# Optimization experiments

Measured on AMD Instinct MI355X. Metric: run time of the kernel, lower is better.

## Reference

```python
import jax, jax.numpy as jnp
import numpy as np
from jax import lax

B, T, FEAT = 8, 512, 128
D_MODEL, D_STATE, D_INNER, DT_RANK = 128, 16, 256, 8
N_LAYERS, NUM_CLASSES = 10, 35
FLAT = 64 * (FEAT // 4)  # 2048


def setup_inputs():
    keys = iter(jax.random.split(jax.random.key(0), 48))
    def nrm(shape, s=0.05):
        return jax.random.normal(next(keys), shape, jnp.float32) * s
    inp = {}
    inp['x'] = jax.random.normal(next(keys), (B, T, FEAT), jnp.float32)
    inp['lengths'] = jax.random.randint(next(keys), (B,), 0, T)
    inp['conv_w1'] = nrm((32, 1, 3, 3)); inp['conv_b1'] = nrm((32,))
    inp['bn1_s'] = 1.0 + nrm((32,)); inp['bn1_b'] = nrm((32,))
    inp['conv_w2'] = nrm((32, 32, 3, 3)); inp['conv_b2'] = nrm((32,))
    inp['bn2_s'] = 1.0 + nrm((32,)); inp['bn2_b'] = nrm((32,))
    inp['conv_w3'] = nrm((64, 32, 3, 3)); inp['conv_b3'] = nrm((64,))
    inp['bn3_s'] = 1.0 + nrm((64,)); inp['bn3_b'] = nrm((64,))
    inp['conv_w4'] = nrm((64, 64, 3, 3)); inp['conv_b4'] = nrm((64,))
    inp['bn4_s'] = 1.0 + nrm((64,)); inp['bn4_b'] = nrm((64,))
    inp['proj_w'] = nrm((D_MODEL, FLAT), 0.02); inp['proj_b'] = nrm((D_MODEL,))
    inp['proj_ln_s'] = jnp.ones((D_MODEL,)); inp['proj_ln_b'] = jnp.zeros((D_MODEL,))
    L = N_LAYERS
    inp['blk_ln_s'] = jnp.ones((L, D_MODEL)); inp['blk_ln_b'] = jnp.zeros((L, D_MODEL))
    inp['in_w'] = nrm((L, 2 * D_INNER, D_MODEL))
    inp['cw'] = nrm((L, D_INNER, 4)); inp['cb'] = nrm((L, D_INNER))
    inp['xp_w'] = nrm((L, DT_RANK + 2 * D_STATE, D_INNER))
    inp['dt_w'] = nrm((L, D_INNER, DT_RANK))
    inp['dt_b'] = nrm((L, D_INNER)) - 4.0  # softplus(-4) ~ 0.018: realistic small dt
    inp['A_log'] = jnp.tile(jnp.log(jnp.arange(1, D_STATE + 1, dtype=jnp.float32))[None, None, :], (L, D_INNER, 1))
    inp['Dp'] = jnp.ones((L, D_INNER))
    inp['out_w'] = nrm((L, D_MODEL, D_INNER))
    inp['pre_ln_s'] = jnp.ones((D_MODEL,)); inp['pre_ln_b'] = jnp.zeros((D_MODEL,))
    inp['cls_w1'] = nrm((D_MODEL // 2, D_MODEL)); inp['cls_b1'] = nrm((D_MODEL // 2,))
    inp['cls_w2'] = nrm((NUM_CLASSES, D_MODEL // 2)); inp['cls_b2'] = nrm((NUM_CLASSES,))
    return inp


def _ln(x, s, b):
    m = jnp.mean(x, -1, keepdims=True)
    v = jnp.mean((x - m) ** 2, -1, keepdims=True)
    return (x - m) * lax.rsqrt(v + 1e-5) * s + b


def _conv2d(x, w, b):
    y = lax.conv_general_dilated(x, w, (1, 1), 'SAME', dimension_numbers=('NCHW', 'OIHW', 'NCHW'))
    return y + b[None, :, None, None]


def _bn(x, s, b):  # eval-mode BatchNorm folded to per-channel affine
    return x * s[None, :, None, None] + b[None, :, None, None]


def _pool(x, kh, kw):
    return lax.reduce_window(x, -jnp.inf, lax.max, (1, 1, kh, kw), (1, 1, kh, kw), 'VALID')


def _mamba(x, in_w, cw, cb, xp_w, dt_w, dt_b, A_log, Dp, out_w):
    bb = x.shape[0]
    xz = jnp.einsum('btd,ed->bte', x, in_w)                  # [B,T,2*d_inner]
    xm, z = jnp.split(xz, 2, axis=-1)
    # causal depthwise conv1d (torch pads both sides by 3 then truncates to T == left-pad 3)
    xc = lax.conv_general_dilated(xm.transpose(0, 2, 1), cw[:, None, :], (1,), [(3, 0)],
                                  dimension_numbers=('NCH', 'OIH', 'NCH'), feature_group_count=D_INNER)
    xc = jax.nn.silu(xc + cb[None, :, None]).transpose(0, 2, 1)  # [B,T,d_inner]
    dbc = jnp.einsum('btd,ed->bte', xc, xp_w)
    dt, Bm, Cm = jnp.split(dbc, [DT_RANK, DT_RANK + D_STATE], axis=-1)
    dt = jax.nn.softplus(jnp.einsum('btr,dr->btd', dt, dt_w) + dt_b)  # [B,T,d_inner]
    A = -jnp.exp(A_log)                                      # [d_inner,d_state]
    dA = jnp.exp(dt[..., None] * A)                          # [B,T,d,n]
    dBu = (dt * xc)[..., None] * Bm[:, :, None, :]           # [B,T,d,n]
    def step(h, inp):
        dA_t, dBu_t, C_t = inp
        h = dA_t * h + dBu_t
        return h, jnp.einsum('bdn,bn->bd', h, C_t)
    h0 = jnp.zeros((bb, D_INNER, D_STATE), x.dtype)
    _, ys = lax.scan(step, h0, (dA.transpose(1, 0, 2, 3), dBu.transpose(1, 0, 2, 3), Cm.transpose(1, 0, 2)))
    y = ys.transpose(1, 0, 2) + Dp * xc
    y = y * jax.nn.silu(z)
    return jnp.einsum('btd,ed->bte', y, out_w)


def _forward(x, lengths, conv_w1, conv_b1, bn1_s, bn1_b, conv_w2, conv_b2, bn2_s, bn2_b,
             conv_w3, conv_b3, bn3_s, bn3_b, conv_w4, conv_b4, bn4_s, bn4_b,
             proj_w, proj_b, proj_ln_s, proj_ln_b, blk_ln_s, blk_ln_b,
             in_w, cw, cb, xp_w, dt_w, dt_b, A_log, Dp, out_w,
             pre_ln_s, pre_ln_b, cls_w1, cls_b1, cls_w2, cls_b2):
    h = x.transpose(0, 2, 1)[:, None]                        # [B,1,F,T]
    h = jax.nn.silu(_bn(_conv2d(h, conv_w1, conv_b1), bn1_s, bn1_b))
    h = jax.nn.silu(_bn(_conv2d(h, conv_w2, conv_b2), bn2_s, bn2_b))
    h = _pool(h, 2, 2)
    h = jax.nn.silu(_bn(_conv2d(h, conv_w3, conv_b3), bn3_s, bn3_b))
    h = jax.nn.silu(_bn(_conv2d(h, conv_w4, conv_b4), bn4_s, bn4_b))
    h = _pool(h, 2, 1)                                       # [B,64,F/4,T/2]
    h = h.transpose(0, 3, 1, 2).reshape(h.shape[0], h.shape[3], -1)  # [B,T',64*F/4]
    h = jax.nn.silu(_ln(jnp.einsum('btf,df->btd', h, proj_w) + proj_b, proj_ln_s, proj_ln_b))
    for i in range(N_LAYERS):
        h = h + _mamba(_ln(h, blk_ln_s[i], blk_ln_b[i]), in_w[i], cw[i], cb[i], xp_w[i],
                       dt_w[i], dt_b[i], A_log[i], Dp[i], out_w[i])
    h = _ln(h, pre_ln_s, pre_ln_b)
    t_lens = jnp.clip(lengths // 2, 1)
    mask = (jnp.arange(h.shape[1])[None, :] < t_lens[:, None]).astype(h.dtype)[..., None]
    pooled = (h * mask).sum(1) / jnp.clip(mask.sum(1), 1.0)
    c = jax.nn.silu(jnp.einsum('bd,hd->bh', pooled, cls_w1) + cls_b1)
    return jnp.einsum('bh,ch->bc', c, cls_w2) + cls_b2


def reference(x, lengths, conv_w1, conv_b1, bn1_s, bn1_b, conv_w2, conv_b2, bn2_s, bn2_b,
              conv_w3, conv_b3, bn3_s, bn3_b, conv_w4, conv_b4, bn4_s, bn4_b,
              proj_w, proj_b, proj_ln_s, proj_ln_b, blk_ln_s, blk_ln_b,
              in_w, cw, cb, xp_w, dt_w, dt_b, A_log, Dp, out_w,
              pre_ln_s, pre_ln_b, cls_w1, cls_b1, cls_w2, cls_b2):
    return _forward(x, lengths, conv_w1, conv_b1, bn1_s, bn1_b, conv_w2, conv_b2, bn2_s, bn2_b,
                    conv_w3, conv_b3, bn3_s, bn3_b, conv_w4, conv_b4, bn4_s, bn4_b,
                    proj_w, proj_b, proj_ln_s, proj_ln_b, blk_ln_s, blk_ln_b,
                    in_w, cw, cb, xp_w, dt_w, dt_b, A_log, Dp, out_w,
                    pre_ln_s, pre_ln_b, cls_w1, cls_b1, cls_w2, cls_b2)
```

## Files before the change

### kernel.cpp

```cpp
#include <hip/hip_runtime.h>
#include <math.h>

#define B_ 8
#define T_ 512
#define FEAT_ 128
#define TP 256
#define DM 128
#define DI 256
#define DS 16
#define DTR 8
#define NL 10

__device__ __forceinline__ float fsilu(float x){ return x / (1.f + __expf(-x)); }
__device__ __forceinline__ float fsoftplus(float x){ return (x > 20.f) ? x : log1pf(__expf(x)); }

__global__ void k_transpose_x(const float* __restrict__ x, float* __restrict__ xT){
  int idx = blockIdx.x*256 + threadIdx.x;
  if(idx >= B_*FEAT_*T_) return;
  int t = idx % T_; int f = (idx/T_) % FEAT_; int b = idx/(T_*FEAT_);
  xT[idx] = x[((size_t)b*T_ + t)*FEAT_ + f];
}

__device__ __forceinline__ void wt_one(const float* __restrict__ w, float* __restrict__ o,
                                       int idx, int CO, int CIN){
  int k = idx % 9; int ci = (idx/9) % CIN; int co = idx/(9*CIN);
  o[((size_t)(ci*(CO>>3) + (co>>3)))*72 + (co&7)*9 + k] = w[idx];
}
__global__ void k_wt_all(const float* __restrict__ w1, const float* __restrict__ w2,
                         const float* __restrict__ w3, const float* __restrict__ w4,
                         float* __restrict__ o1, float* __restrict__ o2,
                         float* __restrict__ o3, float* __restrict__ o4){
  int idx = blockIdx.x*256 + threadIdx.x;
  if(idx < 288){ wt_one(w1, o1, idx, 32, 1); return; }
  idx -= 288;
  if(idx < 9216){ wt_one(w2, o2, idx, 32, 32); return; }
  idx -= 9216;
  if(idx < 18432){ wt_one(w3, o3, idx, 64, 32); return; }
  idx -= 18432;
  if(idx < 36864){ wt_one(w4, o4, idx, 64, 64); return; }
}

template<int CIN, int CO, int CPW, int CIG, int COG>
__global__ __launch_bounds__(256) void k_conv_t4(const float* __restrict__ in,
     const float* __restrict__ wt, const float* __restrict__ cb,
     const float* __restrict__ bs, const float* __restrict__ bb,
     float* __restrict__ out, int H, int W){
  constexpr int NS = CO/CPW;
  __shared__ __align__(16) float tile[CIG*360];
  int tid = threadIdx.x;
  int lane = tid & 63;
  int wav = __builtin_amdgcn_readfirstlane(tid >> 6);
  int wpr = W >> 4, hpr = H >> 4;
  int idx = blockIdx.x;
  int cog = idx % COG; idx /= COG;
  int tj = idx % wpr; idx /= wpr;
  int ti = idx % hpr; int b = idx / hpr;
  int i0 = ti*16, j0 = tj*16;
  int r = lane & 15, cg = lane >> 4;
  int wslot = cog*4 + wav;
  const float* wbase = wt + (size_t)wslot*72;
  float acc[CPW][4] = {};
  for(int cig = 0; cig < CIN; cig += CIG){
    __syncthreads();
    for(int u = tid; u < CIG*324; u += 256){
      int ci = u / 324; int rem = u - ci*324; int rr = rem / 18; int cc = rem - rr*18;
      int gi = i0 - 1 + rr, gj = j0 - 1 + cc;
      float v = 0.f;
      if(gi >= 0 && gi < H && gj >= 0 && gj < W)
        v = in[((size_t)(b*CIN + cig + ci)*H + gi)*W + gj];
      tile[ci*360 + rr*20 + cc] = v;
    }
    __syncthreads();
    for(int ci = 0; ci < CIG; ci++){
      const float4* wp4 = (const float4*)(wbase + (size_t)(cig+ci)*(NS*72));
      float4 w4q[18];
      #pragma unroll
      for(int q=0;q<18;q++) w4q[q] = wp4[q];
      const float* wf = (const float*)w4q;
      #pragma unroll
      for(int kh=0;kh<3;kh++){
        float4 a = *(const float4*)&tile[ci*360 + (r+kh)*20 + cg*4];
        float4 bv = *(const float4*)&tile[ci*360 + (r+kh)*20 + cg*4 + 4];
        float v[6] = {a.x,a.y,a.z,a.w,bv.x,bv.y};
        #pragma unroll
        for(int co=0;co<CPW;co++){
          #pragma unroll
          for(int kw=0;kw<3;kw++){
            float wv = wf[co*9 + kh*3 + kw];
            #pragma unroll
            for(int u2=0;u2<4;u2++)
              acc[co][u2] = fmaf(wv, v[kw+u2], acc[co][u2]);
          }
        }
      }
    }
  }
  int i = i0 + r;
  #pragma unroll
  for(int co=0; co<CPW; co++){
    int c = cog*(4*CPW) + wav*CPW + co;
    float s = bs[c], bias = cb[c]*s + bb[c];
    float4 o;
    o.x = fsilu(acc[co][0]*s + bias);
    o.y = fsilu(acc[co][1]*s + bias);
    o.z = fsilu(acc[co][2]*s + bias);
    o.w = fsilu(acc[co][3]*s + bias);
    *(float4*)&out[((size_t)(b*CO + c)*H + i)*W + j0 + cg*4] = o;
  }
}

__global__ void k_pool2x2(const float* __restrict__ in, float* __restrict__ out,
                          int C, int Hi, int Wi){
  int Ho = Hi>>1, Wo = Wi>>1;
  int total = B_*C*Ho*Wo;
  int idx = blockIdx.x*256 + threadIdx.x;
  if(idx >= total) return;
  int j = idx % Wo; int i = (idx/Wo)%Ho; int c = (idx/(Wo*Ho))%C; int b = idx/(Wo*Ho*C);
  const float* p = in + (((size_t)(b*C+c)*Hi + 2*i)*Wi + 2*j);
  out[idx] = fmaxf(fmaxf(p[0], p[1]), fmaxf(p[Wi], p[Wi+1]));
}

__global__ __launch_bounds__(256) void k_proj(const float* __restrict__ R0,
    const float* __restrict__ W, float* __restrict__ pbuf){
  __shared__ __align__(16) float As[16][33];
  __shared__ __align__(16) float Ws[16][68];
  int tid = threadIdx.x;
  int n0 = blockIdx.x*64, m0 = blockIdx.y*32;
  int kc = blockIdx.z;
  int b = m0 >> 8;
  int t_base = m0 & 255;
  int tx = tid&15, ty = tid>>4;
  float acc[2][4] = {};
  for(int k0=0; k0<256; k0+=16){
    int kg0 = kc*256 + k0;
    if(tid < 128){
      int row = tid>>2, cq = (tid&3)*4;
      #pragma unroll
      for(int c2=0;c2<4;c2++){
        int k = kg0 + cq + c2;
        int c = k>>5, hh = k&31;
        const float* p = R0 + (((size_t)(b*64+c)*64 + 2*hh)*256 + t_base + row);
        As[cq+c2][row] = fmaxf(p[0], p[256]);
      }
    } else {
      int u = tid - 128; int n = u>>1, cq = (u&1)*8;
      const float* wp = W + (size_t)(n0+n)*2048 + kg0 + cq;
      float4 v0 = *(const float4*)wp, v1 = *(const float4*)(wp+4);
      Ws[cq+0][n]=v0.x; Ws[cq+1][n]=v0.y; Ws[cq+2][n]=v0.z; Ws[cq+3][n]=v0.w;
      Ws[cq+4][n]=v1.x; Ws[cq+5][n]=v1.y; Ws[cq+6][n]=v1.z; Ws[cq+7][n]=v1.w;
    }
    __syncthreads();
    #pragma unroll
    for(int kk=0;kk<16;kk++){
      float a0 = As[kk][ty*2+0];
      float a1 = As[kk][ty*2+1];
      float4 w4 = *(const float4*)&Ws[kk][tx*4];
      float wv4[4] = {w4.x,w4.y,w4.z,w4.w};
      #pragma unroll
      for(int j=0;j<4;j++){
        acc[0][j] = fmaf(a0, wv4[j], acc[0][j]);
        acc[1][j] = fmaf(a1, wv4[j], acc[1][j]);
      }
    }
    __syncthreads();
  }
  float* pb = pbuf + (size_t)kc*2048*DM;
  #pragma unroll
  for(int iu=0;iu<2;iu++){
    int m = m0 + ty*2 + iu;
    #pragma unroll
    for(int j=0;j<4;j++){
      int n = n0 + tx*4 + j;
      pb[(size_t)m*DM + n] = acc[iu][j];
    }
  }
}

__global__ void k_lnp(const float* __restrict__ pbuf, const float* __restrict__ bias,
                      const float* __restrict__ g, const float* __restrict__ b,
                      float* __restrict__ out){
  int row = blockIdx.x;
  int t = threadIdx.x;
  float v0 = bias[t], v1 = bias[t+64];
  #pragma unroll
  for(int kc=0;kc<8;kc++){
    const float* p = pbuf + ((size_t)kc*2048 + row)*DM;
    v0 += p[t]; v1 += p[t+64];
  }
  float s = v0 + v1;
  #pragma unroll
  for(int m=32;m>=1;m>>=1) s += __shfl_xor(s, m);
  float mean = s * (1.f/128.f);
  float e0 = v0-mean, e1 = v1-mean;
  float q = e0*e0 + e1*e1;
  #pragma unroll
  for(int m=32;m>=1;m>>=1) q += __shfl_xor(q, m);
  float inv = rsqrtf(q*(1.f/128.f) + 1e-5f);
  float o0 = fsilu(e0*inv*g[t] + b[t]);
  float o1 = fsilu(e1*inv*g[t+64] + b[t+64]);
  float* po = out + (size_t)row*DM;
  po[t] = o0; po[t+64] = o1;
}

template<int SILU>
__global__ void k_ln(const float* __restrict__ in, const float* __restrict__ g,
                     const float* __restrict__ b, float* __restrict__ out){
  int row = blockIdx.x;
  int t = threadIdx.x;
  const float* p = in + (size_t)row*DM;
  float v0 = p[t], v1 = p[t+64];
  float s = v0 + v1;
  #pragma unroll
  for(int m=32;m>=1;m>>=1) s += __shfl_xor(s, m);
  float mean = s * (1.f/128.f);
  float e0 = v0-mean, e1 = v1-mean;
  float q = e0*e0 + e1*e1;
  #pragma unroll
  for(int m=32;m>=1;m>>=1) q += __shfl_xor(q, m);
  float inv = rsqrtf(q*(1.f/128.f) + 1e-5f);
  float o0 = e0*inv*g[t] + b[t];
  float o1 = e1*inv*g[t+64] + b[t+64];
  if(SILU){ o0 = fsilu(o0); o1 = fsilu(o1); }
  float* po = out + (size_t)row*DM;
  po[t] = o0; po[t+64] = o1;
}

__global__ __launch_bounds__(256) void k_lnxz(const float* __restrict__ hbuf,
    const float* __restrict__ g, const float* __restrict__ bb,
    const float* __restrict__ W, float* __restrict__ out){
  __shared__ __align__(16) float lns[32][132];
  __shared__ __align__(16) float Ws[16][68];
  int tid = threadIdx.x;
  int n0 = blockIdx.x*64, m0 = blockIdx.y*32;
  for(int u=tid; u<1024; u+=256){
    int row = u>>5, c4 = (u&31)*4;
    float4 v = *(const float4*)(hbuf + (size_t)(m0+row)*DM + c4);
    lns[row][c4] = v.x; lns[row][c4+1] = v.y; lns[row][c4+2] = v.z; lns[row][c4+3] = v.w;
  }
  __syncthreads();
  {
    int lane = tid & 63, wv = tid >> 6;
    for(int rr = wv; rr < 32; rr += 4){
      float v0 = lns[rr][lane], v1 = lns[rr][lane+64];
      float s = v0+v1;
      #pragma unroll
      for(int mm=32;mm>=1;mm>>=1) s += __shfl_xor(s,mm);
      float mean = s*(1.f/128.f);
      float e0 = v0-mean, e1 = v1-mean;
      float q = e0*e0+e1*e1;
      #pragma unroll
      for(int mm=32;mm>=1;mm>>=1) q += __shfl_xor(q,mm);
      float inv = rsqrtf(q*(1.f/128.f)+1e-5f);
      lns[rr][lane]    = e0*inv*g[lane] + bb[lane];
      lns[rr][lane+64] = e1*inv*g[lane+64] + bb[lane+64];
    }
  }
  __syncthreads();
  int tx = tid&15, ty = tid>>4;
  float acc[2][4] = {};
  for(int k0=0;k0<128;k0+=16){
    {
      int n = tid>>2, c4 = (tid&3)*4;
      float4 v = *(const float4*)(W + (size_t)(n0+n)*DM + k0 + c4);
      Ws[c4+0][n]=v.x; Ws[c4+1][n]=v.y; Ws[c4+2][n]=v.z; Ws[c4+3][n]=v.w;
    }
    __syncthreads();
    #pragma unroll
    for(int kk=0;kk<16;kk++){
      float a0 = lns[ty*2+0][k0+kk];
      float a1 = lns[ty*2+1][k0+kk];
      float4 w4 = *(const float4*)&Ws[kk][tx*4];
      float wv4[4] = {w4.x,w4.y,w4.z,w4.w};
      #pragma unroll
      for(int j=0;j<4;j++){
        acc[0][j] = fmaf(a0, wv4[j], acc[0][j]);
        acc[1][j] = fmaf(a1, wv4[j], acc[1][j]);
      }
    }
    __syncthreads();
  }
  #pragma unroll
  for(int iu=0;iu<2;iu++){
    int m = m0 + ty*2 + iu;
    float* po = out + (size_t)m*512 + n0 + tx*4;
    #pragma unroll
    for(int j=0;j<4;j++) po[j] = acc[iu][j];
  }
}

__global__ __launch_bounds__(256) void k_xproj8(const float* __restrict__ xz,
    const float* __restrict__ cw, const float* __restrict__ cb,
    const float* __restrict__ xpw, const float* __restrict__ dtw,
    const float* __restrict__ dtb_, float* __restrict__ xc_g,
    float* __restrict__ dbc_g, float* __restrict__ dt_g){
  __shared__ float xzs[11][64];
  __shared__ float As[64][9];
  __shared__ float Wp[64][41];
  __shared__ float dtin[8][9];
  __shared__ float dtw_s[256][9];
  int tid = threadIdx.x;
  int row0 = blockIdx.x*8; int b = row0 >> 8; int t0 = row0 & 255;
  int rA = tid & 7, cgA = tid >> 3;
  int dlC = tid & 63, rqC = tid >> 6;
  float acc0 = 0.f, acc1 = 0.f;
  for(int ch=0; ch<4; ch++){
    int d0 = ch*64;
    __syncthreads();
    for(int u=tid; u<11*64; u+=256){
      int rr = u>>6, dl = u&63;
      int t = t0 + rr - 3;
      xzs[rr][dl] = (t >= 0) ? xz[((size_t)(b*TP)+t)*512 + d0 + dl] : 0.f;
    }
    for(int u=tid; u<40*64; u+=256){
      int nn = u>>6, dk = u&63;
      Wp[dk][nn] = xpw[(size_t)nn*DI + d0 + dk];
    }
    __syncthreads();
    {
      float cw0 = cw[(d0+dlC)*4+0], cw1 = cw[(d0+dlC)*4+1];
      float cw2 = cw[(d0+dlC)*4+2], cw3 = cw[(d0+dlC)*4+3];
      float cbv = cb[d0+dlC];
      #pragma unroll
      for(int i=0;i<2;i++){
        int rr = rqC*2 + i;
        float a = cbv;
        a = fmaf(cw0, xzs[rr+0][dlC], a);
        a = fmaf(cw1, xzs[rr+1][dlC], a);
        a = fmaf(cw2, xzs[rr+2][dlC], a);
        a = fmaf(cw3, xzs[rr+3][dlC], a);
        float v = fsilu(a);
        As[dlC][rr] = v;
        xc_g[((size_t)row0 + rr)*DI + d0 + dlC] = v;
      }
    }
    __syncthreads();
    for(int dk=0; dk<64; dk++){
      float a = As[dk][rA];
      acc0 = fmaf(a, Wp[dk][cgA], acc0);
      if(cgA < 8) acc1 = fmaf(a, Wp[dk][cgA+32], acc1);
    }
  }
  if(cgA < 8){
    dtin[rA][cgA] = acc0;
    dbc_g[((size_t)row0 + rA)*40 + cgA + 32] = acc1;
  } else {
    dbc_g[((size_t)row0 + rA)*40 + cgA] = acc0;
  }
  for(int u=tid; u<256*8; u+=256) dtw_s[u>>3][u&7] = dtw[u];
  __syncthreads();
  {
    int d = tid;
    float bias = dtb_[d];
    float w8[8];
    #pragma unroll
    for(int k=0;k<8;k++) w8[k] = dtw_s[d][k];
    #pragma unroll
    for(int r2=0;r2<8;r2++){
      float a = bias;
      #pragma unroll
      for(int k=0;k<8;k++) a = fmaf(dtin[r2][k], w8[k], a);
      dt_g[((size_t)row0 + r2)*DI + d] = fsoftplus(a);
    }
  }
}

__global__ __launch_bounds__(1024) void k_scan3(const float* __restrict__ dtb,
      const float* __restrict__ xc, const float* __restrict__ xz,
      const float* __restrict__ dbc, const float* __restrict__ A_log,
      const float* __restrict__ Dp, float* __restrict__ y){
  __shared__ float dt_s[TP][8], xc_s[TP][8];
  __shared__ float Bs[TP][16], Cs[TP][16];
  __shared__ float Eb[8][128], Pb[8][128];
  int tid = threadIdx.x;
  int c = tid >> 7, gl = (tid >> 4) & 7, n = tid & 15;
  int dblk = blockIdx.x & 31, b = blockIdx.x >> 5;
  int d0 = dblk*8;
  size_t rbase = (size_t)b*TP;
  for(int u=tid; u<TP*8; u+=1024){
    int tt = u>>3, gg = u&7;
    size_t r = rbase + tt;
    dt_s[tt][gg] = dtb[r*DI + d0 + gg];
    xc_s[tt][gg] = xc [r*DI + d0 + gg];
  }
  for(int u=tid; u<TP*16; u+=1024){
    int tt = u>>4, nn = u&15;
    size_t r = rbase + tt;
    Bs[tt][nn] = dbc[r*40 + 8  + nn];
    Cs[tt][nn] = dbc[r*40 + 24 + nn];
  }
  __syncthreads();
  int d = d0 + gl;
  float An = -__expf(A_log[d*DS + n]);
  float h = 0.f, dtsum = 0.f;
  int tA = c*32;
  float yloc[32], ev[32];
  #pragma unroll
  for(int i=0;i<32;i++){
    int t = tA + i;
    float dtv = dt_s[t][gl];
    dtsum += dtv;
    float e = __expf(dtv*An);
    ev[i] = e;
    h = fmaf(e, h, dtv*xc_s[t][gl]*Bs[t][n]);
    float p = h*Cs[t][n];
    p += __shfl_xor(p,1); p += __shfl_xor(p,2);
    p += __shfl_xor(p,4); p += __shfl_xor(p,8);
    yloc[i] = p;
  }
  Eb[c][gl*16+n] = h;
  Pb[c][gl*16+n] = __expf(An*dtsum);
  __syncthreads();
  float g = 0.f;
  for(int cp=0; cp<c; cp++)
    g = fmaf(Pb[cp][gl*16+n], g, Eb[cp][gl*16+n]);
  float Dpd = Dp[d];
  #pragma unroll
  for(int i=0;i<32;i++){
    int t = tA + i;
    g *= ev[i];
    float p = g*Cs[t][n];
    p += __shfl_xor(p,1); p += __shfl_xor(p,2);
    p += __shfl_xor(p,4); p += __shfl_xor(p,8);
    if(n==0){
      float zv = xz[(rbase+t)*512 + DI + d];
      float xcv = xc_s[t][gl];
      y[(rbase+t)*DI + d] = (yloc[i] + p + Dpd*xcv) * fsilu(zv);
    }
  }
}

__global__ __launch_bounds__(256) void k_out16(const float* __restrict__ A,
    const float* __restrict__ W, float* __restrict__ C){
  __shared__ float As[16][17];
  __shared__ __align__(16) float Ws[16][68];
  int tid = threadIdx.x;
  int n0 = blockIdx.x*64, m0 = blockIdx.y*16;
  int tx = tid&15, ty = tid>>4;
  float acc[4] = {};
  for(int k0=0;k0<256;k0+=16){
    {
      int row = tid>>4, kk = tid&15;
      As[kk][row] = A[(size_t)(m0+row)*DI + k0 + kk];
    }
    {
      int n = tid>>2, cq = (tid&3)*4;
      float4 v = *(const float4*)(W + (size_t)(n0+n)*DI + k0 + cq);
      Ws[cq+0][n]=v.x; Ws[cq+1][n]=v.y; Ws[cq+2][n]=v.z; Ws[cq+3][n]=v.w;
    }
    __syncthreads();
    #pragma unroll
    for(int kk=0;kk<16;kk++){
      float a0 = As[kk][ty];
      float4 w4 = *(const float4*)&Ws[kk][tx*4];
      acc[0] = fmaf(a0, w4.x, acc[0]);
      acc[1] = fmaf(a0, w4.y, acc[1]);
      acc[2] = fmaf(a0, w4.z, acc[2]);
      acc[3] = fmaf(a0, w4.w, acc[3]);
    }
    __syncthreads();
  }
  int m = m0 + ty;
  float* cp = &C[(size_t)m*DM + n0 + tx*4];
  cp[0] += acc[0]; cp[1] += acc[1]; cp[2] += acc[2]; cp[3] += acc[3];
}

__global__ void k_head(const float* __restrict__ hln, const int* __restrict__ lengths,
                       const float* __restrict__ w1, const float* __restrict__ b1,
                       const float* __restrict__ w2, const float* __restrict__ b2,
                       float* __restrict__ out){
  __shared__ float pooled[DM];
  __shared__ float cbuf[64];
  int b = blockIdx.x, tid = threadIdx.x;
  int tl = lengths[b] >> 1; if(tl < 1) tl = 1;
  float s = 0.f;
  const float* p = hln + (size_t)b*TP*DM + tid;
  for(int t=0;t<tl;t++) s += p[(size_t)t*DM];
  pooled[tid] = s / (float)tl;
  __syncthreads();
  if(tid < 64){
    float a = b1[tid];
    const float* wp = w1 + tid*DM;
    for(int k=0;k<DM;k++) a = fmaf(pooled[k], wp[k], a);
    cbuf[tid] = fsilu(a);
  }
  __syncthreads();
  if(tid < 35){
    float a = b2[tid];
    const float* wp = w2 + tid*64;
    for(int k=0;k<64;k++) a = fmaf(cbuf[k], wp[k], a);
    out[b*35+tid] = a;
  }
}

extern "C" void kernel_launch(void* const* d_in, const int* in_sizes, int n_in,
                              void* d_out, int out_size, void* d_ws, size_t ws_size,
                              hipStream_t stream){
  (void)in_sizes; (void)n_in; (void)out_size; (void)ws_size;
  const float* x        = (const float*)d_in[0];
  const int*   lengths  = (const int*)  d_in[1];
  const float* conv_w1  = (const float*)d_in[2];  const float* conv_b1 = (const float*)d_in[3];
  const float* bn1_s    = (const float*)d_in[4];  const float* bn1_b   = (const float*)d_in[5];
  const float* conv_w2  = (const float*)d_in[6];  const float* conv_b2 = (const float*)d_in[7];
  const float* bn2_s    = (const float*)d_in[8];  const float* bn2_b   = (const float*)d_in[9];
  const float* conv_w3  = (const float*)d_in[10]; const float* conv_b3 = (const float*)d_in[11];
  const float* bn3_s    = (const float*)d_in[12]; const float* bn3_b   = (const float*)d_in[13];
  const float* conv_w4  = (const float*)d_in[14]; const float* conv_b4 = (const float*)d_in[15];
  const float* bn4_s    = (const float*)d_in[16]; const float* bn4_b   = (const float*)d_in[17];
  const float* proj_w   = (const float*)d_in[18]; const float* proj_b  = (const float*)d_in[19];
  const float* proj_ln_s= (const float*)d_in[20]; const float* proj_ln_b=(const float*)d_in[21];
  const float* blk_ln_s = (const float*)d_in[22]; const float* blk_ln_b =(const float*)d_in[23];
  const float* in_w     = (const float*)d_in[24];
  const float* cw       = (const float*)d_in[25]; const float* cbv     = (const float*)d_in[26];
  const float* xp_w     = (const float*)d_in[27];
  const float* dt_w     = (const float*)d_in[28]; const float* dt_b    = (const float*)d_in[29];
  const float* A_log    = (const float*)d_in[30]; const float* Dp      = (const float*)d_in[31];
  const float* out_w    = (const float*)d_in[32];
  const float* pre_ln_s = (const float*)d_in[33]; const float* pre_ln_b= (const float*)d_in[34];
  const float* cls_w1   = (const float*)d_in[35]; const float* cls_b1  = (const float*)d_in[36];
  const float* cls_w2   = (const float*)d_in[37]; const float* cls_b2  = (const float*)d_in[38];

  float* ws   = (float*)d_ws;
  float* R0   = ws;
  float* R1   = R0 + 16777216;
  float* xT   = R1 + 16777216;
  float* hbuf = xT + 524288;
  float* lnb  = hbuf + 262144;
  float* xzb  = lnb + 262144;
  float* xcb  = xzb + 1048576;
  float* dbcb = xcb + 524288;
  float* dtbb = dbcb + 81920;
  float* yb   = dtbb + 524288;
  float* wt1  = yb + 524288;
  float* wt2  = wt1 + 288;
  float* wt3  = wt2 + 9216;
  float* wt4  = wt3 + 18432;

  k_wt_all<<<254, 256, 0, stream>>>(conv_w1, conv_w2, conv_w3, conv_w4, wt1, wt2, wt3, wt4);

  k_transpose_x<<<2048, 256, 0, stream>>>(x, xT);
  k_conv_t4<1,32,8,1,1><<<8*8*32, 256, 0, stream>>>(xT, wt1, conv_b1, bn1_s, bn1_b, R0, 128, 512);
  k_conv_t4<32,32,8,8,1><<<8*8*32, 256, 0, stream>>>(R0, wt2, conv_b2, bn2_s, bn2_b, R1, 128, 512);
  k_pool2x2<<<(8*32*64*256)/256, 256, 0, stream>>>(R1, R0, 32, 128, 512);
  k_conv_t4<32,64,8,8,2><<<8*4*16*2, 256, 0, stream>>>(R0, wt3, conv_b3, bn3_s, bn3_b, R1, 64, 256);
  k_conv_t4<64,64,8,8,2><<<8*4*16*2, 256, 0, stream>>>(R1, wt4, conv_b4, bn4_s, bn4_b, R0, 64, 256);

  {
    dim3 g(2, 64, 8);
    k_proj<<<g, 256, 0, stream>>>(R0, proj_w, R1);
  }
  k_lnp<<<2048, 64, 0, stream>>>(R1, proj_b, proj_ln_s, proj_ln_b, hbuf);

  for(int i=0;i<NL;i++){
    { dim3 g(8, 64);
      k_lnxz<<<g, 256, 0, stream>>>(hbuf, blk_ln_s + i*DM, blk_ln_b + i*DM,
                                    in_w + (size_t)i*512*DM, xzb); }
    k_xproj8<<<256, 256, 0, stream>>>(xzb, cw + (size_t)i*DI*4, cbv + i*DI,
                                      xp_w + (size_t)i*40*DI, dt_w + (size_t)i*DI*DTR,
                                      dt_b + i*DI, xcb, dbcb, dtbb);
    k_scan3<<<256, 1024, 0, stream>>>(dtbb, xcb, xzb, dbcb, A_log + (size_t)i*DI*DS, Dp + i*DI, yb);
    { dim3 g(2, 128);
      k_out16<<<g, 256, 0, stream>>>(yb, out_w + (size_t)i*DM*DI, hbuf); }
  }

  k_ln<0><<<2048, 64, 0, stream>>>(hbuf, pre_ln_s, pre_ln_b, lnb);
  k_head<<<8, 128, 0, stream>>>(lnb, lengths, cls_w1, cls_b1, cls_w2, cls_b2, (float*)d_out);
}
```

Baseline: 1.279 ms.

## Fuse block LayerNorm, in-projection, conv and x-projection into one kernel

Merges the per-layer LN+in_proj GEMM kernel with the depthwise conv/x_proj/dt kernel. Each block now recomputes LN and the in-projection for 8 rows plus a 3-row causal halo and keeps the x half in shared memory. Only the z half goes to a narrower global buffer, which removes the round trip of the full 512-wide xz tensor. The final LayerNorm is also folded into the pooling head kernel. The trade-off is redundant halo GEMM work, only 256 blocks, and weights read directly from global memory per thread instead of a shared tiled GEMM.

After: 1.339 ms. 4.7% more time.

```diff
diff --git a/kernel.cpp b/kernel.cpp
--- a/kernel.cpp
+++ b/kernel.cpp
@@ -202,46 +202,31 @@
   po[t] = o0; po[t+64] = o1;
 }
 
-template<int SILU>
-__global__ void k_ln(const float* __restrict__ in, const float* __restrict__ g,
-                     const float* __restrict__ b, float* __restrict__ out){
-  int row = blockIdx.x;
-  int t = threadIdx.x;
-  const float* p = in + (size_t)row*DM;
-  float v0 = p[t], v1 = p[t+64];
-  float s = v0 + v1;
-  #pragma unroll
-  for(int m=32;m>=1;m>>=1) s += __shfl_xor(s, m);
-  float mean = s * (1.f/128.f);
-  float e0 = v0-mean, e1 = v1-mean;
-  float q = e0*e0 + e1*e1;
-  #pragma unroll
-  for(int m=32;m>=1;m>>=1) q += __shfl_xor(q, m);
-  float inv = rsqrtf(q*(1.f/128.f) + 1e-5f);
-  float o0 = e0*inv*g[t] + b[t];
-  float o1 = e1*inv*g[t+64] + b[t+64];
-  if(SILU){ o0 = fsilu(o0); o1 = fsilu(o1); }
-  float* po = out + (size_t)row*DM;
-  po[t] = o0; po[t+64] = o1;
-}
-
-__global__ __launch_bounds__(256) void k_lnxz(const float* __restrict__ hbuf,
+__global__ __launch_bounds__(256) void k_min(const float* __restrict__ hb,
     const float* __restrict__ g, const float* __restrict__ bb,
-    const float* __restrict__ W, float* __restrict__ out){
-  __shared__ __align__(16) float lns[32][132];
-  __shared__ __align__(16) float Ws[16][68];
+    const float* __restrict__ W,
+    const float* __restrict__ cw, const float* __restrict__ cb,
+    const float* __restrict__ xpw, const float* __restrict__ dtw,
+    const float* __restrict__ dtb_,
+    float* __restrict__ zb, float* __restrict__ xc_g,
+    float* __restrict__ dbc_g, float* __restrict__ dt_g){
+  __shared__ __align__(16) float lns[11][132];
+  __shared__ __align__(16) float xms[11][260];
+  __shared__ __align__(16) float xcs[8][260];
+  __shared__ float Wp[64][41];
+  __shared__ float dtin[8][9];
   int tid = threadIdx.x;
-  int n0 = blockIdx.x*64, m0 = blockIdx.y*32;
-  for(int u=tid; u<1024; u+=256){
-    int row = u>>5, c4 = (u&31)*4;
-    float4 v = *(const float4*)(hbuf + (size_t)(m0+row)*DM + c4);
-    lns[row][c4] = v.x; lns[row][c4+1] = v.y; lns[row][c4+2] = v.z; lns[row][c4+3] = v.w;
+  int row0 = blockIdx.x*8; int b = row0 >> 8; int t0 = row0 & 255;
+  for(int u=tid; u<11*128; u+=256){
+    int r = u>>7, col = u&127;
+    int t = t0 - 3 + r;
+    lns[r][col] = (t >= 0) ? hb[((size_t)(b*TP)+t)*DM + col] : 0.f;
   }
   __syncthreads();
   {
     int lane = tid & 63, wv = tid >> 6;
-    for(int rr = wv; rr < 32; rr += 4){
-      float v0 = lns[rr][lane], v1 = lns[rr][lane+64];
+    for(int r = wv; r < 11; r += 4){
+      float v0 = lns[r][lane], v1 = lns[r][lane+64];
       float s = v0+v1;
       #pragma unroll
       for(int mm=32;mm>=1;mm>>=1) s += __shfl_xor(s,mm);
@@ -251,121 +236,111 @@
       #pragma unroll
       for(int mm=32;mm>=1;mm>>=1) q += __shfl_xor(q,mm);
       float inv = rsqrtf(q*(1.f/128.f)+1e-5f);
-      lns[rr][lane]    = e0*inv*g[lane] + bb[lane];
-      lns[rr][lane+64] = e1*inv*g[lane+64] + bb[lane+64];
-    }
-  }
-  __syncthreads();
-  int tx = tid&15, ty = tid>>4;
-  float acc[2][4] = {};
-  for(int k0=0;k0<128;k0+=16){
-    {
-      int n = tid>>2, c4 = (tid&3)*4;
-      float4 v = *(const float4*)(W + (size_t)(n0+n)*DM + k0 + c4);
-      Ws[c4+0][n]=v.x; Ws[c4+1][n]=v.y; Ws[c4+2][n]=v.z; Ws[c4+3][n]=v.w;
-    }
-    __syncthreads();
-    #pragma unroll
-    for(int kk=0;kk<16;kk++){
-      float a0 = lns[ty*2+0][k0+kk];
-      float a1 = lns[ty*2+1][k0+kk];
-      float4 w4 = *(const float4*)&Ws[kk][tx*4];
-      float wv4[4] = {w4.x,w4.y,w4.z,w4.w};
-      #pragma unroll
-      for(int j=0;j<4;j++){
-        acc[0][j] = fmaf(a0, wv4[j], acc[0][j]);
-        acc[1][j] = fmaf(a1, wv4[j], acc[1][j]);
-      }
-    }
-    __syncthreads();
-  }
-  #pragma unroll
-  for(int iu=0;iu<2;iu++){
-    int m = m0 + ty*2 + iu;
-    float* po = out + (size_t)m*512 + n0 + tx*4;
-    #pragma unroll
-    for(int j=0;j<4;j++) po[j] = acc[iu][j];
-  }
-}
-
-__global__ __launch_bounds__(256) void k_xproj8(const float* __restrict__ xz,
-    const float* __restrict__ cw, const float* __restrict__ cb,
-    const float* __restrict__ xpw, const float* __restrict__ dtw,
-    const float* __restrict__ dtb_, float* __restrict__ xc_g,
-    float* __restrict__ dbc_g, float* __restrict__ dt_g){
-  __shared__ float xzs[11][64];
-  __shared__ float As[64][9];
-  __shared__ float Wp[64][41];
-  __shared__ float dtin[8][9];
-  __shared__ float dtw_s[256][9];
-  int tid = threadIdx.x;
-  int row0 = blockIdx.x*8; int b = row0 >> 8; int t0 = row0 & 255;
-  int rA = tid & 7, cgA = tid >> 3;
-  int dlC = tid & 63, rqC = tid >> 6;
-  float acc0 = 0.f, acc1 = 0.f;
-  for(int ch=0; ch<4; ch++){
-    int d0 = ch*64;
-    __syncthreads();
-    for(int u=tid; u<11*64; u+=256){
-      int rr = u>>6, dl = u&63;
-      int t = t0 + rr - 3;
-      xzs[rr][dl] = (t >= 0) ? xz[((size_t)(b*TP)+t)*512 + d0 + dl] : 0.f;
-    }
-    for(int u=tid; u<40*64; u+=256){
-      int nn = u>>6, dk = u&63;
-      Wp[dk][nn] = xpw[(size_t)nn*DI + d0 + dk];
-    }
-    __syncthreads();
-    {
-      float cw0 = cw[(d0+dlC)*4+0], cw1 = cw[(d0+dlC)*4+1];
-      float cw2 = cw[(d0+dlC)*4+2], cw3 = cw[(d0+dlC)*4+3];
-      float cbv = cb[d0+dlC];
-      #pragma unroll
-      for(int i=0;i<2;i++){
-        int rr = rqC*2 + i;
-        float a = cbv;
-        a = fmaf(cw0, xzs[rr+0][dlC], a);
-        a = fmaf(cw1, xzs[rr+1][dlC], a);
-        a = fmaf(cw2, xzs[rr+2][dlC], a);
-        a = fmaf(cw3, xzs[rr+3][dlC], a);
-        float v = fsilu(a);
-        As[dlC][rr] = v;
-        xc_g[((size_t)row0 + rr)*DI + d0 + dlC] = v;
-      }
-    }
-    __syncthreads();
-    for(int dk=0; dk<64; dk++){
-      float a = As[dk][rA];
-      acc0 = fmaf(a, Wp[dk][cgA], acc0);
-      if(cgA < 8) acc1 = fmaf(a, Wp[dk][cgA+32], acc1);
-    }
-  }
-  if(cgA < 8){
-    dtin[rA][cgA] = acc0;
-    dbc_g[((size_t)row0 + rA)*40 + cgA + 32] = acc1;
-  } else {
-    dbc_g[((size_t)row0 + rA)*40 + cgA] = acc0;
-  }
-  for(int u=tid; u<256*8; u+=256) dtw_s[u>>3][u&7] = dtw[u];
+      lns[r][lane]    = e0*inv*g[lane] + bb[lane];
+      lns[r][lane+64] = e1*inv*g[lane+64] + bb[lane+64];
+    }
+  }
+  __syncthreads();
+  {
+    int c2 = tid & 63, chq = tid >> 6;
+    int colb = chq*64 + c2;
+    #pragma unroll
+    for(int pass=0; pass<2; pass++){
+      const float* wp = W + (size_t)(pass*256 + colb)*DM;
+      float acc[11];
+      #pragma unroll
+      for(int r=0;r<11;r++) acc[r]=0.f;
+      for(int kb=0; kb<128; kb+=32){
+        float wreg[32];
+        #pragma unroll
+        for(int q=0;q<8;q++){
+          float4 w4 = *(const float4*)(wp + kb + q*4);
+          wreg[q*4]=w4.x; wreg[q*4+1]=w4.y; wreg[q*4+2]=w4.z; wreg[q*4+3]=w4.w;
+        }
+        #pragma unroll
+        for(int r=0;r<11;r++){
+          #pragma unroll
+          for(int q=0;q<8;q++){
+            float4 a4 = *(const float4*)&lns[r][kb+q*4];
+            acc[r] = fmaf(a4.x, wreg[q*4+0], acc[r]);
+            acc[r] = fmaf(a4.y, wreg[q*4+1], acc[r]);
+            acc[r] = fmaf(a4.z, wreg[q*4+2], acc[r]);
+            acc[r] = fmaf(a4.w, wreg[q*4+3], acc[r]);
+          }
+        }
+      }
+      if(pass==0){
+        #pragma unroll
+        for(int r=0;r<11;r++)
+          xms[r][colb] = (t0-3+r >= 0) ? acc[r] : 0.f;
+      } else {
+        #pragma unroll
+        for(int r=3;r<11;r++)
+          zb[((size_t)(row0 + r-3))*DI + colb] = acc[r];
+      }
+    }
+  }
+  __syncthreads();
+  {
+    int d = tid;
+    float4 cw4 = *(const float4*)&cw[d*4];
+    float cbv = cb[d];
+    #pragma unroll
+    for(int r2=0;r2<8;r2++){
+      float a = cbv;
+      a = fmaf(cw4.x, xms[r2+0][d], a);
+      a = fmaf(cw4.y, xms[r2+1][d], a);
+      a = fmaf(cw4.z, xms[r2+2][d], a);
+      a = fmaf(cw4.w, xms[r2+3][d], a);
+      float v = fsilu(a);
+      xcs[r2][d] = v;
+      xc_g[((size_t)(row0+r2))*DI + d] = v;
+    }
+  }
+  {
+    int row = tid>>5, cg = tid&31;
+    float a0 = 0.f, a1 = 0.f;
+    for(int ch2=0; ch2<4; ch2++){
+      __syncthreads();
+      for(int u=tid; u<40*64; u+=256){
+        int nn = u>>6, dk = u&63;
+        Wp[dk][nn] = xpw[(size_t)nn*DI + ch2*64 + dk];
+      }
+      __syncthreads();
+      #pragma unroll 8
+      for(int dk=0; dk<64; dk++){
+        float a = xcs[row][ch2*64+dk];
+        a0 = fmaf(a, Wp[dk][cg], a0);
+        if(cg < 8) a1 = fmaf(a, Wp[dk][cg+32], a1);
+      }
+    }
+    if(cg < 8){
+      dtin[row][cg] = a0;
+      dbc_g[((size_t)(row0+row))*40 + 32 + cg] = a1;
+    } else {
+      dbc_g[((size_t)(row0+row))*40 + cg] = a0;
+    }
+  }
   __syncthreads();
   {
     int d = tid;
     float bias = dtb_[d];
-    float w8[8];
-    #pragma unroll
-    for(int k=0;k<8;k++) w8[k] = dtw_s[d][k];
+    float4 wa = *(const float4*)&dtw[d*8];
+    float4 wb = *(const float4*)&dtw[d*8+4];
     #pragma unroll
     for(int r2=0;r2<8;r2++){
       float a = bias;
-      #pragma unroll
-      for(int k=0;k<8;k++) a = fmaf(dtin[r2][k], w8[k], a);
-      dt_g[((size_t)row0 + r2)*DI + d] = fsoftplus(a);
+      a = fmaf(dtin[r2][0], wa.x, a); a = fmaf(dtin[r2][1], wa.y, a);
+      a = fmaf(dtin[r2][2], wa.z, a); a = fmaf(dtin[r2][3], wa.w, a);
+      a = fmaf(dtin[r2][4], wb.x, a); a = fmaf(dtin[r2][5], wb.y, a);
+      a = fmaf(dtin[r2][6], wb.z, a); a = fmaf(dtin[r2][7], wb.w, a);
+      dt_g[((size_t)(row0+r2))*DI + d] = fsoftplus(a);
     }
   }
 }
 
 __global__ __launch_bounds__(1024) void k_scan3(const float* __restrict__ dtb,
-      const float* __restrict__ xc, const float* __restrict__ xz,
+      const float* __restrict__ xc, const float* __restrict__ zb,
       const float* __restrict__ dbc, const float* __restrict__ A_log,
       const float* __restrict__ Dp, float* __restrict__ y){
   __shared__ float dt_s[TP][8], xc_s[TP][8];
@@ -422,7 +397,7 @@
     p += __shfl_xor(p,1); p += __shfl_xor(p,2);
     p += __shfl_xor(p,4); p += __shfl_xor(p,8);
     if(n==0){
-      float zv = xz[(rbase+t)*512 + DI + d];
+      float zv = zb[(rbase+t)*DI + d];
       float xcv = xc_s[t][gl];
       y[(rbase+t)*DI + d] = (yloc[i] + p + Dpd*xcv) * fsilu(zv);
     }
@@ -464,18 +439,37 @@
   cp[0] += acc[0]; cp[1] += acc[1]; cp[2] += acc[2]; cp[3] += acc[3];
 }
 
-__global__ void k_head(const float* __restrict__ hln, const int* __restrict__ lengths,
-                       const float* __restrict__ w1, const float* __restrict__ b1,
-                       const float* __restrict__ w2, const float* __restrict__ b2,
-                       float* __restrict__ out){
+__global__ __launch_bounds__(256) void k_head2(const float* __restrict__ h,
+    const int* __restrict__ lengths, const float* __restrict__ g,
+    const float* __restrict__ bv, const float* __restrict__ w1,
+    const float* __restrict__ b1, const float* __restrict__ w2,
+    const float* __restrict__ b2, float* __restrict__ out){
+  __shared__ float pp[4][128];
   __shared__ float pooled[DM];
   __shared__ float cbuf[64];
   int b = blockIdx.x, tid = threadIdx.x;
+  int lane = tid & 63, wv = tid >> 6;
   int tl = lengths[b] >> 1; if(tl < 1) tl = 1;
-  float s = 0.f;
-  const float* p = hln + (size_t)b*TP*DM + tid;
-  for(int t=0;t<tl;t++) s += p[(size_t)t*DM];
-  pooled[tid] = s / (float)tl;
+  float p0 = 0.f, p1 = 0.f;
+  for(int t = wv; t < tl; t += 4){
+    const float* row = h + ((size_t)(b*TP)+t)*DM;
+    float v0 = row[lane], v1 = row[lane+64];
+    float s = v0+v1;
+    #pragma unroll
+    for(int mm=32;mm>=1;mm>>=1) s += __shfl_xor(s,mm);
+    float mean = s*(1.f/128.f);
+    float e0 = v0-mean, e1 = v1-mean;
+    float q = e0*e0+e1*e1;
+    #pragma unroll
+    for(int mm=32;mm>=1;mm>>=1) q += __shfl_xor(q,mm);
+    float inv = rsqrtf(q*(1.f/128.f)+1e-5f);
+    p0 += e0*inv*g[lane] + bv[lane];
+    p1 += e1*inv*g[lane+64] + bv[lane+64];
+  }
+  pp[wv][lane] = p0; pp[wv][lane+64] = p1;
+  __syncthreads();
+  if(tid < 128)
+    pooled[tid] = (pp[0][tid]+pp[1][tid]+pp[2][tid]+pp[3][tid]) / (float)tl;
   __syncthreads();
   if(tid < 64){
     float a = b1[tid];
@@ -525,8 +519,8 @@
   float* xT   = R1 + 16777216;
   float* hbuf = xT + 524288;
   float* lnb  = hbuf + 262144;
-  float* xzb  = lnb + 262144;
-  float* xcb  = xzb + 1048576;
+  float* zb   = lnb + 262144;
+  float* xcb  = zb + 1048576;
   float* dbcb = xcb + 524288;
   float* dtbb = dbcb + 81920;
   float* yb   = dtbb + 524288;
@@ -545,23 +539,22 @@
   k_conv_t4<64,64,8,8,2><<<8*4*16*2, 256, 0, stream>>>(R1, wt4, conv_b4, bn4_s, bn4_b, R0, 64, 256);
 
   {
-    dim3 g(2, 64, 8);
-    k_proj<<<g, 256, 0, stream>>>(R0, proj_w, R1);
+    dim3 gd(2, 64, 8);
+    k_proj<<<gd, 256, 0, stream>>>(R0, proj_w, R1);
   }
   k_lnp<<<2048, 64, 0, stream>>>(R1, proj_b, proj_ln_s, proj_ln_b, hbuf);
 
   for(int i=0;i<NL;i++){
-    { dim3 g(8, 64);
-      k_lnxz<<<g, 256, 0, stream>>>(hbuf, blk_ln_s + i*DM, blk_ln_b + i*DM,
-                                    in_w + (size_t)i*512*DM, xzb); }
-    k_xproj8<<<256, 256, 0, stream>>>(xzb, cw + (size_t)i*DI*4, cbv + i*DI,
-                                      xp_w + (size_t)i*40*DI, dt_w + (size_t)i*DI*DTR,
-                                      dt_b + i*DI, xcb, dbcb, dtbb);
-    k_scan3<<<256, 1024, 0, stream>>>(dtbb, xcb, xzb, dbcb, A_log + (size_t)i*DI*DS, Dp + i*DI, yb);
-    { dim3 g(2, 128);
-      k_out16<<<g, 256, 0, stream>>>(yb, out_w + (size_t)i*DM*DI, hbuf); }
-  }
-
-  k_ln<0><<<2048, 64, 0, stream>>>(hbuf, pre_ln_s, pre_ln_b, lnb);
-  k_head<<<8, 128, 0, stream>>>(lnb, lengths, cls_w1, cls_b1, cls_w2, cls_b2, (float*)d_out);
-}
+    k_min<<<256, 256, 0, stream>>>(hbuf, blk_ln_s + i*DM, blk_ln_b + i*DM,
+                                   in_w + (size_t)i*512*DM,
+                                   cw + (size_t)i*DI*4, cbv + i*DI,
+                                   xp_w + (size_t)i*40*DI, dt_w + (size_t)i*DI*DTR,
+                                   dt_b + i*DI, zb, xcb, dbcb, dtbb);
+    k_scan3<<<256, 1024, 0, stream>>>(dtbb, xcb, zb, dbcb, A_log + (size_t)i*DI*DS, Dp + i*DI, yb);
+    { dim3 gd(2, 128);
+      k_out16<<<gd, 256, 0, stream>>>(yb, out_w + (size_t)i*DM*DI, hbuf); }
+  }
+
+  k_head2<<<8, 256, 0, stream>>>(hbuf, lengths, pre_ln_s, pre_ln_b,
+                                 cls_w1, cls_b1, cls_w2, cls_b2, (float*)d_out);
+}
```
